# Kernel tuning notes

Measured on AMD Instinct MI355X. Metric: run time of the kernel, lower is better.

The kernel has to match this reference:

```python
import jax, jax.numpy as jnp
import numpy as np

N, H2, T = 64, 1024, 512  # num steps/documents, 2*hidden_dim, tokens per step
EPS = 1e-12  # torch F.normalize eps


def setup_inputs() -> dict:
    key = jax.random.key(0)
    k1, k2, k3, k4 = jax.random.split(key, 4)
    return {
        "hidden_states": jax.random.normal(k1, (N, H2, T), dtype=jnp.float32),
        "W_attention": jax.random.normal(k2, (H2, H2), dtype=jnp.float32),
        "bias_attention": jax.random.normal(k3, (H2,), dtype=jnp.float32),
        "u_w0": jax.random.normal(k4, (H2,), dtype=jnp.float32),
    }


def reference(hidden_states, W_attention, bias_attention, u_w0):
    n = hidden_states.shape[0]

    # Sequential recurrence on u_w: u_w <- normalize(u_w @ W^T + b), updated
    # BEFORE being used at each step i. Collect the post-update value per step.
    def step(u, _):
        u_new = u @ W_attention.T + bias_attention
        u_new = u_new / jnp.maximum(jnp.linalg.norm(u_new), EPS)
        return u_new, u_new

    _, u_ws = jax.lax.scan(step, u_w0, None, length=n)  # (N, 2H)

    # u_it = tanh(h_i^T W^T + b) for all steps, batched: (N, T, 2H)
    u_it = jnp.tanh(jnp.einsum('ndt,ed->nte', hidden_states, W_attention)
                    + bias_attention)

    # attention scores per step, softmax over the T axis (torch Softmax(dim=0)
    # on a (T,1) column)
    scores = jnp.einsum('nte,ne->nt', u_it, u_ws)  # (N, T)
    a = jax.nn.softmax(scores, axis=1)

    # weighted sum s_i = h_i @ a_i -> stacked as rows: (N, 2H)
    s = jnp.einsum('ndt,nt->nd', hidden_states, a)
    return s
```

## Files before the change

kernel.cpp:

```cpp
#include <hip/hip_runtime.h>
#include <cstdint>
#include <cstddef>

#define H2 1024
#define TT 512
#define NSTEPS 64
#define RBLK 32
#define RTHR 512
#define PREBLK 224
#define TOTBLK 256
#define NTILES 2048u

using floatx4 = __attribute__((__ext_vector_type__(4))) float;
using half8   = __attribute__((__ext_vector_type__(8))) _Float16;
using half4   = __attribute__((__ext_vector_type__(4))) _Float16;
typedef unsigned long long u64;

__device__ __forceinline__ float tanh_fast(float x) {
  return 1.0f - 2.0f / (__expf(2.0f * x) + 1.0f);
}

#define GLDS16(gp, lp)                                                         \
  __builtin_amdgcn_global_load_lds(                                            \
      (const __attribute__((address_space(1))) void*)(gp),                     \
      (__attribute__((address_space(3))) void*)(lp), 16, 0, 0)

__global__ __launch_bounds__(RTHR, 1) void fused_kernel(
    const float* __restrict__ W, const float* __restrict__ bias,
    const float* __restrict__ u0, float* __restrict__ vbuf,
    float* __restrict__ norm2, _Float16* __restrict__ Wh,
    const float* __restrict__ h, _Float16* __restrict__ hhT,
    float* __restrict__ scores, unsigned* __restrict__ ctrs) {
  __shared__ __align__(16) char smem[33792];
  int tid = threadIdx.x;
  unsigned* done  = ctrs;
  unsigned* queue = ctrs + 16;

  if (blockIdx.x < RBLK) {
    float* ub = (float*)smem;
    float* bredn = (float*)(smem + 8192);
    int w = tid >> 6, l = tid & 63;
    int r0 = blockIdx.x * RBLK + w * 4;

    floatx4 wreg[16];
    float blv[4];
#pragma unroll
    for (int p = 0; p < 4; ++p) {
      const float* wr = W + ((size_t)(r0 + p) << 10) + 4 * l;
#pragma unroll
      for (int j = 0; j < 4; ++j)
        wreg[p * 4 + j] = *(const floatx4*)(wr + 256 * j);
      blv[p] = bias[r0 + p];
    }
#pragma unroll
    for (int j = 0; j < 16; ++j) asm volatile("" : "+v"(wreg[j]));

    for (int i = 0; i < NSTEPS; ++i) {
      float* cb = ub + (i & 1) * 1024;
      float rs;
      if (i == 0) {
        if (w == 0) {
#pragma unroll
          for (int j = 0; j < 4; ++j) {
            floatx4 v = *((const floatx4*)u0 + l + 64 * j);
            *(floatx4*)(cb + 4 * l + 256 * j) = v;
          }
        }
        __syncthreads();
        rs = 1.0f;
      } else {
        if (w == 0) {
          const u64* src = (const u64*)(vbuf + ((size_t)(i - 1) << 10)) + l;
          u64 v[8];
          for (;;) {
            bool ok = true;
#pragma unroll
            for (int j = 0; j < 8; ++j) {
              v[j] = __hip_atomic_load(src + 64 * j, __ATOMIC_RELAXED,
                                       __HIP_MEMORY_SCOPE_AGENT);
              ok &= ((unsigned)(v[j] & 0xFFFFFFFFu) != 0xFFFFFFFFu) &
                    ((unsigned)(v[j] >> 32) != 0xFFFFFFFFu);
            }
            if (__all(ok)) break;
            __builtin_amdgcn_s_sleep(1);
          }
          float sq = 0.f;
#pragma unroll
          for (int j = 0; j < 8; ++j) {
            *(u64*)(cb + 2 * l + 128 * j) = v[j];
            float f0 =
                __builtin_bit_cast(float, (unsigned)(v[j] & 0xFFFFFFFFu));
            float f1 = __builtin_bit_cast(float, (unsigned)(v[j] >> 32));
            sq += f0 * f0 + f1 * f1;
          }
#pragma unroll
          for (int off = 1; off <= 32; off <<= 1)
            sq += __shfl_xor(sq, off, 64);
          if (l == 0) bredn[i & 1] = sq;
        }
        __syncthreads();
        float nrm = bredn[i & 1];
        rs = 1.0f / fmaxf(sqrtf(nrm), 1e-12f);
        if (blockIdx.x == 0 && tid == 64) {
          unsigned nb = __builtin_bit_cast(unsigned, nrm);
          __hip_atomic_store((unsigned*)(norm2 + (i - 1)), nb,
                             __ATOMIC_RELAXED, __HIP_MEMORY_SCOPE_AGENT);
        }
      }

      float acc0 = 0.f, acc1 = 0.f, acc2 = 0.f, acc3 = 0.f;
#pragma unroll
      for (int j = 0; j < 4; ++j) {
        floatx4 zv = *(const floatx4*)(cb + 256 * j + 4 * l);
        floatx4 w0 = wreg[0 * 4 + j], w1 = wreg[1 * 4 + j];
        floatx4 w2 = wreg[2 * 4 + j], w3 = wreg[3 * 4 + j];
        acc0 += w0.x * zv.x + w0.y * zv.y + w0.z * zv.z + w0.w * zv.w;
        acc1 += w1.x * zv.x + w1.y * zv.y + w1.z * zv.z + w1.w * zv.w;
        acc2 += w2.x * zv.x + w2.y * zv.y + w2.z * zv.z + w2.w * zv.w;
        acc3 += w3.x * zv.x + w3.y * zv.y + w3.z * zv.z + w3.w * zv.w;
      }
#pragma unroll
      for (int off = 1; off <= 32; off <<= 1) {
        acc0 += __shfl_xor(acc0, off, 64);
        acc1 += __shfl_xor(acc1, off, 64);
        acc2 += __shfl_xor(acc2, off, 64);
        acc3 += __shfl_xor(acc3, off, 64);
      }
      if (l == 0) {
        float y0 = acc0 * rs + blv[0], y1 = acc1 * rs + blv[1];
        float y2 = acc2 * rs + blv[2], y3 = acc3 * rs + blv[3];
        u64 a01 = ((u64)__builtin_bit_cast(unsigned, y1) << 32) |
                  (u64)__builtin_bit_cast(unsigned, y0);
        u64 a23 = ((u64)__builtin_bit_cast(unsigned, y3) << 32) |
                  (u64)__builtin_bit_cast(unsigned, y2);
        u64* dst = (u64*)(vbuf + ((size_t)i << 10) + r0);
        __hip_atomic_store(dst, a01, __ATOMIC_RELAXED,
                           __HIP_MEMORY_SCOPE_AGENT);
        __hip_atomic_store(dst + 1, a23, __ATOMIC_RELAXED,
                           __HIP_MEMORY_SCOPE_AGENT);
      }
    }

    if (blockIdx.x == 0 && (tid >> 6) == 0) {
      int l2 = tid & 63;
      const u64* src = (const u64*)(vbuf + ((size_t)(NSTEPS - 1) << 10)) + l2;
      u64 v[8];
      for (;;) {
        bool ok = true;
#pragma unroll
        for (int j = 0; j < 8; ++j) {
          v[j] = __hip_atomic_load(src + 64 * j, __ATOMIC_RELAXED,
                                   __HIP_MEMORY_SCOPE_AGENT);
          ok &= ((unsigned)(v[j] & 0xFFFFFFFFu) != 0xFFFFFFFFu) &
                ((unsigned)(v[j] >> 32) != 0xFFFFFFFFu);
        }
        if (__all(ok)) break;
        __builtin_amdgcn_s_sleep(1);
      }
      float sq = 0.f;
#pragma unroll
      for (int j = 0; j < 8; ++j) {
        float f0 = __builtin_bit_cast(float, (unsigned)(v[j] & 0xFFFFFFFFu));
        float f1 = __builtin_bit_cast(float, (unsigned)(v[j] >> 32));
        sq += f0 * f0 + f1 * f1;
      }
#pragma unroll
      for (int off = 1; off <= 32; off <<= 1) sq += __shfl_xor(sq, off, 64);
      if (l2 == 0) {
        unsigned nb = __builtin_bit_cast(unsigned, sq);
        __hip_atomic_store((unsigned*)(norm2 + (NSTEPS - 1)), nb,
                           __ATOMIC_RELAXED, __HIP_MEMORY_SCOPE_AGENT);
      }
    }
    __syncthreads();
  } else {
    int pb = blockIdx.x - RBLK;

    const floatx4* Wv = (const floatx4*)W;
    for (int idx = pb * RTHR + tid; idx < H2 * H2 / 4; idx += PREBLK * RTHR) {
      floatx4 v = Wv[idx];
      half4 o = {(_Float16)v.x, (_Float16)v.y, (_Float16)v.z, (_Float16)v.w};
      __hip_atomic_store((u64*)Wh + idx, __builtin_bit_cast(u64, o),
                         __ATOMIC_RELAXED, __HIP_MEMORY_SCOPE_AGENT);
    }

    int sub = tid >> 8, ltid = tid & 255;
    float(*tile)[65] = (float(*)[65])(smem + sub * 16640);
    int dr = ltid >> 4, tc = (ltid & 15) << 2;
    int tr = ltid >> 3, seg = ltid & 7;
    for (int base = pb * 2; base < 8192; base += PREBLK * 2) {
      int tidx = base + sub;
      bool act = tidx < 8192;
      int n = tidx >> 7, rem = tidx & 127;
      int d0 = (rem & 15) << 6, t0 = ((rem >> 4) & 7) << 6;
      if (act) {
        const float* hb = h + ((size_t)n * H2 + d0) * TT + t0;
#pragma unroll
        for (int p = 0; p < 4; ++p) {
          floatx4 v = *(const floatx4*)(hb + (size_t)(dr + p * 16) * TT + tc);
          tile[dr + p * 16][tc] = v.x;
          tile[dr + p * 16][tc + 1] = v.y;
          tile[dr + p * 16][tc + 2] = v.z;
          tile[dr + p * 16][tc + 3] = v.w;
        }
      }
      __syncthreads();
      if (act) {
        _Float16* ob = hhT + ((size_t)n * TT + t0) * H2 + d0;
#pragma unroll
        for (int p = 0; p < 2; ++p) {
          int t = tr + p * 32;
          union { half8 v; u64 u[2]; } hu;
#pragma unroll
          for (int u = 0; u < 8; ++u) hu.v[u] = (_Float16)tile[seg * 8 + u][t];
          u64* op = (u64*)(ob + (size_t)t * H2 + seg * 8);
          __hip_atomic_store(op, hu.u[0], __ATOMIC_RELAXED,
                             __HIP_MEMORY_SCOPE_AGENT);
          __hip_atomic_store(op + 1, hu.u[1], __ATOMIC_RELAXED,
                             __HIP_MEMORY_SCOPE_AGENT);
        }
      }
      __syncthreads();
    }
    asm volatile("s_waitcnt vmcnt(0)" ::: "memory");
    __syncthreads();
    if (tid == 0)
      __hip_atomic_fetch_add(done, 1u, __ATOMIC_RELEASE,
                             __HIP_MEMORY_SCOPE_AGENT);
  }

  if (tid == 0) {
    while (__hip_atomic_load(done, __ATOMIC_ACQUIRE,
                             __HIP_MEMORY_SCOPE_AGENT) < (unsigned)PREBLK)
      __builtin_amdgcn_s_sleep(2);
  }
  __syncthreads();

  int half = tid >> 8, tid2 = tid & 255;
  _Float16* Ash = (_Float16*)(smem + half * 16384);
  _Float16* Bsh = Ash + 4096;
  unsigned* tslot = (unsigned*)(smem + 32768);

  int lane = tid2 & 63, w2 = tid2 >> 6;
  int q = lane >> 4, m = lane & 15;
  int eoff = (w2 & 1) * 64, toff = (w2 >> 1) * 64;
  int rl = lane >> 2, kseg = lane & 3;
  _Float16* lA0 = Ash + (w2 * 32) * 32;
  _Float16* lA1 = lA0 + 16 * 32;
  _Float16* lB0 = Bsh + (w2 * 32) * 32;
  _Float16* lB1 = lB0 + 16 * 32;

  for (;;) {
    if (tid == 0) {
      unsigned q0 = atomicAdd(queue, 2u);
      tslot[0] = q0;
      tslot[1] = q0 + 1u;
    }
    __syncthreads();
    if (tslot[0] >= NTILES) break;
    unsigned tau = tslot[half];
    int n = (int)(tau >> 5);
    int rem = (int)(tau & 31u);
    int e_base = (rem & 7) << 7, t_base = (rem >> 3) << 7;

    const _Float16* gA0 =
        Wh + (((size_t)(e_base + w2 * 32 + rl)) << 10) + kseg * 8;
    const _Float16* gA1 = gA0 + ((size_t)16 << 10);
    const _Float16* gB0 = hhT + ((size_t)n << 19) +
                          (((size_t)(t_base + w2 * 32 + rl)) << 10) + kseg * 8;
    const _Float16* gB1 = gB0 + ((size_t)16 << 10);

    floatx4 zero = {0.f, 0.f, 0.f, 0.f};
    floatx4 acc[4][4];
#pragma unroll
    for (int i = 0; i < 4; ++i)
#pragma unroll
      for (int j = 0; j < 4; ++j) acc[i][j] = zero;

    for (int k0 = 0; k0 < H2; k0 += 32) {
      GLDS16(gA0 + k0, lA0);
      GLDS16(gA1 + k0, lA1);
      GLDS16(gB0 + k0, lB0);
      GLDS16(gB1 + k0, lB1);
      __syncthreads();

      half8 af[4], bf[4];
#pragma unroll
      for (int i = 0; i < 4; ++i)
        af[i] = *(const half8*)&Ash[(eoff + i * 16 + m) * 32 + q * 8];
#pragma unroll
      for (int j = 0; j < 4; ++j)
        bf[j] = *(const half8*)&Bsh[(toff + j * 16 + m) * 32 + q * 8];
#pragma unroll
      for (int i = 0; i < 4; ++i)
#pragma unroll
        for (int j = 0; j < 4; ++j)
          acc[i][j] = __builtin_amdgcn_mfma_f32_16x16x32_f16(af[i], bf[j],
                                                             acc[i][j], 0, 0, 0);
      __syncthreads();
    }

    float* uloc = (float*)Ash;
    float* bloc = uloc + 128;
    if (tid2 < 128) {
      float nn;
      for (;;) {
        unsigned b = __hip_atomic_load((const unsigned*)(norm2 + n),
                                       __ATOMIC_RELAXED,
                                       __HIP_MEMORY_SCOPE_AGENT);
        if (b != 0xFFFFFFFFu) {
          nn = __builtin_bit_cast(float, b);
          break;
        }
        __builtin_amdgcn_s_sleep(1);
      }
      float rsn = 1.0f / fmaxf(sqrtf(nn), 1e-12f);
      const unsigned* vp =
          (const unsigned*)(vbuf + ((size_t)n << 10) + e_base) + tid2;
      float vv;
      for (;;) {
        unsigned b =
            __hip_atomic_load(vp, __ATOMIC_RELAXED, __HIP_MEMORY_SCOPE_AGENT);
        if (b != 0xFFFFFFFFu) {
          vv = __builtin_bit_cast(float, b);
          break;
        }
        __builtin_amdgcn_s_sleep(1);
      }
      uloc[tid2] = vv * rsn;
      bloc[tid2] = bias[e_base + tid2];
    }
    __syncthreads();

    float part[4] = {0.f, 0.f, 0.f, 0.f};
#pragma unroll
    for (int i = 0; i < 4; ++i) {
#pragma unroll
      for (int reg = 0; reg < 4; ++reg) {
        int el = eoff + i * 16 + q * 4 + reg;
        float ubv = uloc[el];
        float bbv = bloc[el];
#pragma unroll
        for (int j = 0; j < 4; ++j) {
          float y = acc[i][j][reg] + bbv;
          part[j] += tanh_fast(y) * ubv;
        }
      }
    }
#pragma unroll
    for (int j = 0; j < 4; ++j) {
      part[j] += __shfl_xor(part[j], 16, 64);
      part[j] += __shfl_xor(part[j], 32, 64);
      if (lane < 16) {
        int t = t_base + toff + j * 16 + lane;
        atomicAdd(&scores[(size_t)n * TT + t], part[j]);
      }
    }
    __syncthreads();
  }
}

__global__ __launch_bounds__(256) void out_kernel(
    const float* __restrict__ h, const float* __restrict__ scores,
    float* __restrict__ out) {
  int n = blockIdx.y;
  int ds = blockIdx.x;
  int tid = threadIdx.x;
  int w = tid >> 6, lane = tid & 63;

  __shared__ float sa[TT];
  __shared__ float wred[8];

  float s0 = scores[(size_t)n * TT + tid];
  float s1 = scores[(size_t)n * TT + 256 + tid];

  float mx = fmaxf(s0, s1);
#pragma unroll
  for (int off = 32; off >= 1; off >>= 1) mx = fmaxf(mx, __shfl_xor(mx, off, 64));
  if (lane == 0) wred[w] = mx;
  __syncthreads();
  mx = fmaxf(fmaxf(wred[0], wred[1]), fmaxf(wred[2], wred[3]));

  float e0 = __expf(s0 - mx);
  float e1 = __expf(s1 - mx);
  float ssum = e0 + e1;
#pragma unroll
  for (int off = 32; off >= 1; off >>= 1) ssum += __shfl_xor(ssum, off, 64);
  if (lane == 0) wred[4 + w] = ssum;
  __syncthreads();
  ssum = wred[4] + wred[5] + wred[6] + wred[7];
  float inv = 1.0f / ssum;
  sa[tid] = e0 * inv;
  sa[tid + 256] = e1 * inv;
  __syncthreads();

  int d0 = ds * 64 + w * 16;
  const float4* hb = reinterpret_cast<const float4*>(h + (size_t)n * H2 * TT);
#pragma unroll 1
  for (int rr = 0; rr < 16; ++rr) {
    int d = d0 + rr;
    const float4* hr = hb + (size_t)d * (TT / 4);
    float4 a4 = hr[lane];
    float4 b4 = hr[64 + lane];
    int t0 = 4 * lane;
    float acc = a4.x * sa[t0] + a4.y * sa[t0 + 1] + a4.z * sa[t0 + 2] +
                a4.w * sa[t0 + 3] + b4.x * sa[256 + t0] +
                b4.y * sa[256 + t0 + 1] + b4.z * sa[256 + t0 + 2] +
                b4.w * sa[256 + t0 + 3];
#pragma unroll
    for (int off = 1; off <= 32; off <<= 1) acc += __shfl_xor(acc, off, 64);
    if (lane == 0) out[(size_t)n * H2 + d] = acc;
  }
}

extern "C" void kernel_launch(void* const* d_in, const int* in_sizes, int n_in,
                              void* d_out, int out_size, void* d_ws, size_t ws_size,
                              hipStream_t stream) {
  const float* h    = (const float*)d_in[0];
  const float* W    = (const float*)d_in[1];
  const float* bias = (const float*)d_in[2];
  const float* u0   = (const float*)d_in[3];
  float* out = (float*)d_out;

  float* wsf    = (float*)d_ws;
  float* norm2  = wsf;
  float* scores = wsf + 64;
  float* vbuf   = wsf + 64 + NSTEPS * TT;
  unsigned* ctrs = (unsigned*)(vbuf + (size_t)NSTEPS * H2);
  float* after = (float*)(ctrs + 32);
  _Float16* Wh  = (_Float16*)after;
  _Float16* hhT = Wh + (size_t)H2 * H2;

  hipMemsetAsync(norm2, 0xFF, 64 * sizeof(float), stream);
  hipMemsetAsync(scores, 0, (size_t)NSTEPS * TT * sizeof(float), stream);
  hipMemsetAsync(vbuf, 0xFF, (size_t)NSTEPS * H2 * sizeof(float), stream);
  hipMemsetAsync(ctrs, 0, 32 * sizeof(unsigned), stream);

  {
    const float* Wp = W; const float* bp = bias; const float* up = u0;
    float* vp = vbuf; float* np = norm2;
    _Float16* whp = Wh; const float* hp = h; _Float16* htp = hhT;
    float* sp = scores; unsigned* cp = ctrs;
    void* kargs[] = {&Wp, &bp, &up, &vp, &np, &whp, &hp, &htp, &sp, &cp};
    hipLaunchCooperativeKernel((void*)fused_kernel, dim3(TOTBLK), dim3(RTHR),
                               kargs, 0, stream);
  }

  out_kernel<<<dim3(16, 64), dim3(256), 0, stream>>>(h, scores, out);

  (void)in_sizes; (void)n_in; (void)out_size; (void)ws_size;
}
```

Before: 489.1 us.

## Triple-buffer GEMM loads with XOR-swizzled LDS and fuse softmax-output stage

The tile GEMM loop now uses a three-stage LDS ring. Global-to-LDS loads are issued two k-steps ahead and gated by vmcnt waits instead of two full barriers per step, and the LDS layout is XOR-swizzled to reduce bank conflicts. The separate softmax/weighted-sum kernel is folded into the cooperative kernel as a work queue. Each item waits on a per-document completion counter, so output work for early documents overlaps the remaining GEMM tiles and one launch is removed. LDS use grows to about 96KB per block, and correctness now depends on the counters and the manual waitcnt logic.

```diff
diff --git a/kernel.cpp b/kernel.cpp
--- a/kernel.cpp
+++ b/kernel.cpp
@@ -10,6 +10,7 @@
 #define PREBLK 224
 #define TOTBLK 256
 #define NTILES 2048u
+#define NOUT 512u
 
 using floatx4 = __attribute__((__ext_vector_type__(4))) float;
 using half8   = __attribute__((__ext_vector_type__(8))) _Float16;
@@ -30,11 +31,14 @@
     const float* __restrict__ u0, float* __restrict__ vbuf,
     float* __restrict__ norm2, _Float16* __restrict__ Wh,
     const float* __restrict__ h, _Float16* __restrict__ hhT,
-    float* __restrict__ scores, unsigned* __restrict__ ctrs) {
-  __shared__ __align__(16) char smem[33792];
+    float* __restrict__ scores, float* __restrict__ out,
+    unsigned* __restrict__ ctrs) {
+  __shared__ __align__(16) char smem[98432];
   int tid = threadIdx.x;
-  unsigned* done  = ctrs;
-  unsigned* queue = ctrs + 16;
+  unsigned* done    = ctrs;
+  unsigned* queue   = ctrs + 16;
+  unsigned* donecnt = ctrs + 32;
+  unsigned* outq    = ctrs + 96;
 
   if (blockIdx.x < RBLK) {
     float* ub = (float*)smem;
@@ -113,10 +117,10 @@
       for (int j = 0; j < 4; ++j) {
         floatx4 zv = *(const floatx4*)(cb + 256 * j + 4 * l);
         floatx4 w0 = wreg[0 * 4 + j], w1 = wreg[1 * 4 + j];
-        floatx4 w2 = wreg[2 * 4 + j], w3 = wreg[3 * 4 + j];
+        floatx4 w2v = wreg[2 * 4 + j], w3 = wreg[3 * 4 + j];
         acc0 += w0.x * zv.x + w0.y * zv.y + w0.z * zv.z + w0.w * zv.w;
         acc1 += w1.x * zv.x + w1.y * zv.y + w1.z * zv.z + w1.w * zv.w;
-        acc2 += w2.x * zv.x + w2.y * zv.y + w2.z * zv.z + w2.w * zv.w;
+        acc2 += w2v.x * zv.x + w2v.y * zv.y + w2v.z * zv.z + w2v.w * zv.w;
         acc3 += w3.x * zv.x + w3.y * zv.y + w3.z * zv.z + w3.w * zv.w;
       }
 #pragma unroll
@@ -237,18 +241,15 @@
   __syncthreads();
 
   int half = tid >> 8, tid2 = tid & 255;
-  _Float16* Ash = (_Float16*)(smem + half * 16384);
-  _Float16* Bsh = Ash + 4096;
-  unsigned* tslot = (unsigned*)(smem + 32768);
+  _Float16* Hsh = (_Float16*)(smem) + half * 24576;
+  unsigned* tslot = (unsigned*)(smem + 98304);
 
   int lane = tid2 & 63, w2 = tid2 >> 6;
   int q = lane >> 4, m = lane & 15;
   int eoff = (w2 & 1) * 64, toff = (w2 >> 1) * 64;
   int rl = lane >> 2, kseg = lane & 3;
-  _Float16* lA0 = Ash + (w2 * 32) * 32;
-  _Float16* lA1 = lA0 + 16 * 32;
-  _Float16* lB0 = Bsh + (w2 * 32) * 32;
-  _Float16* lB1 = lB0 + 16 * 32;
+  int ksegx = kseg ^ (rl & 3);
+  int xq = q ^ (m & 3);
 
   for (;;) {
     if (tid == 0) {
@@ -264,10 +265,10 @@
     int e_base = (rem & 7) << 7, t_base = (rem >> 3) << 7;
 
     const _Float16* gA0 =
-        Wh + (((size_t)(e_base + w2 * 32 + rl)) << 10) + kseg * 8;
+        Wh + (((size_t)(e_base + w2 * 32 + rl)) << 10) + ksegx * 8;
     const _Float16* gA1 = gA0 + ((size_t)16 << 10);
     const _Float16* gB0 = hhT + ((size_t)n << 19) +
-                          (((size_t)(t_base + w2 * 32 + rl)) << 10) + kseg * 8;
+                          (((size_t)(t_base + w2 * 32 + rl)) << 10) + ksegx * 8;
     const _Float16* gB1 = gB0 + ((size_t)16 << 10);
 
     floatx4 zero = {0.f, 0.f, 0.f, 0.f};
@@ -277,30 +278,53 @@
 #pragma unroll
       for (int j = 0; j < 4; ++j) acc[i][j] = zero;
 
-    for (int k0 = 0; k0 < H2; k0 += 32) {
-      GLDS16(gA0 + k0, lA0);
-      GLDS16(gA1 + k0, lA1);
-      GLDS16(gB0 + k0, lB0);
-      GLDS16(gB1 + k0, lB1);
-      __syncthreads();
-
+    {
+      _Float16* b0 = Hsh + (w2 * 32) * 32;
+      GLDS16(gA0, b0);
+      GLDS16(gA1, b0 + 512);
+      GLDS16(gB0, b0 + 4096);
+      GLDS16(gB1, b0 + 4096 + 512);
+      _Float16* b1 = Hsh + 8192 + (w2 * 32) * 32;
+      GLDS16(gA0 + 32, b1);
+      GLDS16(gA1 + 32, b1 + 512);
+      GLDS16(gB0 + 32, b1 + 4096);
+      GLDS16(gB1 + 32, b1 + 4096 + 512);
+    }
+#pragma unroll 1
+    for (int kk = 0; kk < 32; ++kk) {
+      if (kk < 31)
+        asm volatile("s_waitcnt vmcnt(4)" ::: "memory");
+      else
+        asm volatile("s_waitcnt vmcnt(0)" ::: "memory");
+      __builtin_amdgcn_s_barrier();
+      __builtin_amdgcn_sched_barrier(0);
+      const _Float16* Abuf = Hsh + (kk % 3) * 8192;
+      const _Float16* Bbuf = Abuf + 4096;
       half8 af[4], bf[4];
 #pragma unroll
       for (int i = 0; i < 4; ++i)
-        af[i] = *(const half8*)&Ash[(eoff + i * 16 + m) * 32 + q * 8];
+        af[i] = *(const half8*)&Abuf[(eoff + i * 16 + m) * 32 + xq * 8];
 #pragma unroll
       for (int j = 0; j < 4; ++j)
-        bf[j] = *(const half8*)&Bsh[(toff + j * 16 + m) * 32 + q * 8];
+        bf[j] = *(const half8*)&Bbuf[(toff + j * 16 + m) * 32 + xq * 8];
+      if (kk + 2 < 32) {
+        _Float16* nb = Hsh + ((kk + 2) % 3) * 8192 + (w2 * 32) * 32;
+        GLDS16(gA0 + (kk + 2) * 32, nb);
+        GLDS16(gA1 + (kk + 2) * 32, nb + 512);
+        GLDS16(gB0 + (kk + 2) * 32, nb + 4096);
+        GLDS16(gB1 + (kk + 2) * 32, nb + 4096 + 512);
+      }
+      __builtin_amdgcn_sched_barrier(0);
 #pragma unroll
       for (int i = 0; i < 4; ++i)
 #pragma unroll
         for (int j = 0; j < 4; ++j)
           acc[i][j] = __builtin_amdgcn_mfma_f32_16x16x32_f16(af[i], bf[j],
                                                              acc[i][j], 0, 0, 0);
-      __syncthreads();
-    }
-
-    float* uloc = (float*)Ash;
+    }
+    __syncthreads();
+
+    float* uloc = (float*)Hsh;
     float* bloc = uloc + 128;
     if (tid2 < 128) {
       float nn;
@@ -357,59 +381,76 @@
       }
     }
     __syncthreads();
+    if (tid2 == 0)
+      __hip_atomic_fetch_add(donecnt + n, 1u, __ATOMIC_RELEASE,
+                             __HIP_MEMORY_SCOPE_AGENT);
   }
-}
-
-__global__ __launch_bounds__(256) void out_kernel(
-    const float* __restrict__ h, const float* __restrict__ scores,
-    float* __restrict__ out) {
-  int n = blockIdx.y;
-  int ds = blockIdx.x;
-  int tid = threadIdx.x;
-  int w = tid >> 6, lane = tid & 63;
-
-  __shared__ float sa[TT];
-  __shared__ float wred[8];
-
-  float s0 = scores[(size_t)n * TT + tid];
-  float s1 = scores[(size_t)n * TT + 256 + tid];
-
-  float mx = fmaxf(s0, s1);
-#pragma unroll
-  for (int off = 32; off >= 1; off >>= 1) mx = fmaxf(mx, __shfl_xor(mx, off, 64));
-  if (lane == 0) wred[w] = mx;
-  __syncthreads();
-  mx = fmaxf(fmaxf(wred[0], wred[1]), fmaxf(wred[2], wred[3]));
-
-  float e0 = __expf(s0 - mx);
-  float e1 = __expf(s1 - mx);
-  float ssum = e0 + e1;
-#pragma unroll
-  for (int off = 32; off >= 1; off >>= 1) ssum += __shfl_xor(ssum, off, 64);
-  if (lane == 0) wred[4 + w] = ssum;
-  __syncthreads();
-  ssum = wred[4] + wred[5] + wred[6] + wred[7];
-  float inv = 1.0f / ssum;
-  sa[tid] = e0 * inv;
-  sa[tid + 256] = e1 * inv;
-  __syncthreads();
-
-  int d0 = ds * 64 + w * 16;
-  const float4* hb = reinterpret_cast<const float4*>(h + (size_t)n * H2 * TT);
+
+  {
+    float* sa = (float*)smem;
+    float* red = sa + 512;
+    unsigned* oslot = (unsigned*)(sa + 528);
+    int w = tid >> 6, lane = tid & 63;
+
+    for (;;) {
+      if (tid == 0) *oslot = atomicAdd(outq, 1u);
+      __syncthreads();
+      unsigned u = *oslot;
+      if (u >= NOUT) break;
+      int n = (int)(u >> 3), dblk = (int)(u & 7u);
+
+      if (tid == 0) {
+        while (__hip_atomic_load(donecnt + n, __ATOMIC_ACQUIRE,
+                                 __HIP_MEMORY_SCOPE_AGENT) < 32u)
+          __builtin_amdgcn_s_sleep(1);
+      }
+      __syncthreads();
+
+      float s = __builtin_bit_cast(
+          float, __hip_atomic_load((const unsigned*)(scores + (size_t)n * TT) +
+                                       tid,
+                                   __ATOMIC_RELAXED, __HIP_MEMORY_SCOPE_AGENT));
+      float mx = s;
+#pragma unroll
+      for (int off = 32; off >= 1; off >>= 1)
+        mx = fmaxf(mx, __shfl_xor(mx, off, 64));
+      if (lane == 0) red[w] = mx;
+      __syncthreads();
+      mx = red[0];
+#pragma unroll
+      for (int k2 = 1; k2 < 8; ++k2) mx = fmaxf(mx, red[k2]);
+      float e = __expf(s - mx);
+      float ssum = e;
+#pragma unroll
+      for (int off = 32; off >= 1; off >>= 1) ssum += __shfl_xor(ssum, off, 64);
+      if (lane == 0) red[8 + w] = ssum;
+      __syncthreads();
+      ssum = 0.f;
+#pragma unroll
+      for (int k2 = 0; k2 < 8; ++k2) ssum += red[8 + k2];
+      sa[tid] = e * (1.0f / ssum);
+      __syncthreads();
+
+      int d0 = dblk * 128 + w * 16;
+      const float4* hb =
+          reinterpret_cast<const float4*>(h + (size_t)n * H2 * TT);
 #pragma unroll 1
-  for (int rr = 0; rr < 16; ++rr) {
-    int d = d0 + rr;
-    const float4* hr = hb + (size_t)d * (TT / 4);
-    float4 a4 = hr[lane];
-    float4 b4 = hr[64 + lane];
-    int t0 = 4 * lane;
-    float acc = a4.x * sa[t0] + a4.y * sa[t0 + 1] + a4.z * sa[t0 + 2] +
-                a4.w * sa[t0 + 3] + b4.x * sa[256 + t0] +
-                b4.y * sa[256 + t0 + 1] + b4.z * sa[256 + t0 + 2] +
-                b4.w * sa[256 + t0 + 3];
-#pragma unroll
-    for (int off = 1; off <= 32; off <<= 1) acc += __shfl_xor(acc, off, 64);
-    if (lane == 0) out[(size_t)n * H2 + d] = acc;
+      for (int rr = 0; rr < 16; ++rr) {
+        int d = d0 + rr;
+        const float4* hr = hb + (size_t)d * (TT / 4);
+        float4 a4 = hr[lane];
+        float4 b4 = hr[64 + lane];
+        int t0 = 4 * lane;
+        float acc = a4.x * sa[t0] + a4.y * sa[t0 + 1] + a4.z * sa[t0 + 2] +
+                    a4.w * sa[t0 + 3] + b4.x * sa[256 + t0] +
+                    b4.y * sa[256 + t0 + 1] + b4.z * sa[256 + t0 + 2] +
+                    b4.w * sa[256 + t0 + 3];
+#pragma unroll
+        for (int off = 1; off <= 32; off <<= 1) acc += __shfl_xor(acc, off, 64);
+        if (lane == 0) out[(size_t)n * H2 + d] = acc;
+      }
+      __syncthreads();
+    }
   }
 }
 
@@ -427,26 +468,24 @@
   float* scores = wsf + 64;
   float* vbuf   = wsf + 64 + NSTEPS * TT;
   unsigned* ctrs = (unsigned*)(vbuf + (size_t)NSTEPS * H2);
-  float* after = (float*)(ctrs + 32);
+  float* after = (float*)(ctrs + 128);
   _Float16* Wh  = (_Float16*)after;
   _Float16* hhT = Wh + (size_t)H2 * H2;
 
   hipMemsetAsync(norm2, 0xFF, 64 * sizeof(float), stream);
   hipMemsetAsync(scores, 0, (size_t)NSTEPS * TT * sizeof(float), stream);
   hipMemsetAsync(vbuf, 0xFF, (size_t)NSTEPS * H2 * sizeof(float), stream);
-  hipMemsetAsync(ctrs, 0, 32 * sizeof(unsigned), stream);
+  hipMemsetAsync(ctrs, 0, 128 * sizeof(unsigned), stream);
 
   {
     const float* Wp = W; const float* bp = bias; const float* up = u0;
     float* vp = vbuf; float* np = norm2;
     _Float16* whp = Wh; const float* hp = h; _Float16* htp = hhT;
-    float* sp = scores; unsigned* cp = ctrs;
-    void* kargs[] = {&Wp, &bp, &up, &vp, &np, &whp, &hp, &htp, &sp, &cp};
+    float* sp = scores; float* op = out; unsigned* cp = ctrs;
+    void* kargs[] = {&Wp, &bp, &up, &vp, &np, &whp, &hp, &htp, &sp, &op, &cp};
     hipLaunchCooperativeKernel((void*)fused_kernel, dim3(TOTBLK), dim3(RTHR),
                                kargs, 0, stream);
   }
 
-  out_kernel<<<dim3(16, 64), dim3(256), 0, stream>>>(h, scores, out);
-
   (void)in_sizes; (void)n_in; (void)out_size; (void)ws_size;
 }
```

Measured after the change: 504.0 us. 3.0% more time.
